# Kernel tuning notes

Measured on AMD Instinct MI355X. Metric: run time of the kernel, lower is better.

Reference implementation:

```python
import jax, jax.numpy as jnp
import numpy as np

N_NODES = 50000
N_EDGES = 1600000
D_IN = 256
HEADS = 4
SUB_IN = 64   # generate_sub_head_nums(256, 4) -> [64, 64, 64, 64]
SUB_H = 64    # hidden_dim // head_num


def setup_inputs() -> dict:
    key = jax.random.key(0)
    k1, k2, k3 = jax.random.split(key, 3)
    x = jax.random.normal(k1, (N_NODES, D_IN), dtype=jnp.float32)
    edge_index = jax.random.randint(k2, (2, N_EDGES), 0, N_NODES, dtype=jnp.int64)
    # per-head GCNConv weights: glorot-ish scale
    W = jax.random.normal(k3, (HEADS, SUB_IN, SUB_H), dtype=jnp.float32) * (1.0 / np.sqrt(SUB_IN))
    b = jnp.zeros((HEADS, SUB_H), dtype=jnp.float32)
    return {"x": x, "edge_index": edge_index, "W": W, "b": b}


def _gcn_aggregate(x_sub, edge_index, n_nodes):
    """Symmetric-normalized aggregation with self-loops: D^-1/2 (A+I) D^-1/2 x_sub."""
    row, col = edge_index[0], edge_index[1]          # source -> target
    loops = jnp.arange(n_nodes, dtype=row.dtype)
    row2 = jnp.concatenate([row, loops])
    col2 = jnp.concatenate([col, loops])
    deg = jax.ops.segment_sum(jnp.ones_like(col2, dtype=x_sub.dtype), col2,
                              num_segments=n_nodes)
    dinv = jnp.where(deg > 0, jax.lax.rsqrt(deg), 0.0)
    norm = dinv[row2] * dinv[col2]                   # [E+N]
    msgs = x_sub[row2] * norm[:, None]               # [E+N, SUB_IN] gather
    return jax.ops.segment_sum(msgs, col2, num_segments=n_nodes)  # [N, SUB_IN] scatter


def reference(x, edge_index, W, b):
    n = x.shape[0]
    # Faithful to source bug: `start` never advances, so every head reads x[:, 0:SUB_IN].
    x0 = x[:, :SUB_IN]                               # [N, 64], shared by all heads
    # aggregation is linear -> aggregate once, then apply per-head linear (same math as GCNConv(xW))
    agg = _gcn_aggregate(x0, edge_index, n)          # [N, 64]
    heads = jax.nn.relu(jnp.einsum('nf,hfo->nho', agg, W) + b[None, :, :])  # [N, H, SUB_H]
    x_cat = heads.reshape(n, HEADS * SUB_H)          # concat over heads along last dim
    return x_cat, heads
```

## Files before the change

### kernel.cpp

```cpp
#include <hip/hip_runtime.h>
#include <hip/hip_bf16.h>

#define NNODES 50000
#define NEDGES 1600000
#define NBIN2  1564
#define CAPB2  1440
#define SCAP   320
#define OVFCAP 65536
#define BCHUNK 2000
#define NBBLK  800

__device__ __forceinline__ float bf2f(unsigned short u) {
    union { unsigned int i; float f; } x; x.i = ((unsigned int)u) << 16; return x.f;
}

__global__ __launch_bounds__(256) void k_bin(const int* __restrict__ edges,
                                             int* __restrict__ bincur,
                                             int* __restrict__ ovfcnt,
                                             int* __restrict__ ovf,
                                             int* __restrict__ binned) {
    __shared__ int pk[BCHUNK];
    __shared__ int hist[NBIN2];
    __shared__ int gbase[NBIN2];
    __shared__ int lcnt[NBIN2];
    int t = threadIdx.x;
    int e0 = blockIdx.x * BCHUNK;
    unsigned xcd;
    asm volatile("s_getreg_b32 %0, hwreg(HW_REG_XCC_ID)" : "=s"(xcd));
    xcd &= 7;
    for (int i = t; i < NBIN2; i += 256) { hist[i] = 0; lcnt[i] = 0; }
    __syncthreads();
    for (int i = t * 4; i < BCHUNK; i += 1024) {
        int4 r4 = *(const int4*)&edges[e0 + i];
        int4 c4 = *(const int4*)&edges[NEDGES + e0 + i];
        int b0 = c4.x >> 5, b1 = c4.y >> 5, b2 = c4.z >> 5, b3 = c4.w >> 5;
        pk[i + 0] = r4.x | ((c4.x & 31) << 16) | (b0 << 21);
        pk[i + 1] = r4.y | ((c4.y & 31) << 16) | (b1 << 21);
        pk[i + 2] = r4.z | ((c4.z & 31) << 16) | (b2 << 21);
        pk[i + 3] = r4.w | ((c4.w & 31) << 16) | (b3 << 21);
        atomicAdd(&hist[b0], 1);
        atomicAdd(&hist[b1], 1);
        atomicAdd(&hist[b2], 1);
        atomicAdd(&hist[b3], 1);
    }
    __syncthreads();
    for (int i = t; i < NBIN2; i += 256) {
        int h = hist[i];
        gbase[i] = (h > 0) ? atomicAdd(&bincur[xcd * NBIN2 + i], h) : 0;
    }
    __syncthreads();
    for (int i = t; i < BCHUNK; i += 256) {
        int v = pk[i];
        int bin = ((unsigned)v) >> 21;
        int p = gbase[bin] + atomicAdd(&lcnt[bin], 1);
        if (p < SCAP) {
            binned[(xcd * NBIN2 + bin) * SCAP + p] = v;
        } else {
            int op = atomicAdd(ovfcnt, 1);
            if (op < OVFCAP) ovf[op] = v;
        }
    }
}

__global__ __launch_bounds__(256) void k_sortbin(const int* __restrict__ bincur,
                                                 const int* __restrict__ binned,
                                                 const int* __restrict__ ovfcnt,
                                                 const int* __restrict__ ovf,
                                                 const float* __restrict__ x,
                                                 int* __restrict__ rowptr,
                                                 int* __restrict__ cntn,
                                                 float* __restrict__ dinv,
                                                 unsigned short* __restrict__ x0s,
                                                 int* __restrict__ csr) {
    __shared__ int h[32];
    __shared__ int off[32];
    __shared__ int cur[32];
    __shared__ float dv[32];
    __shared__ int slen[8];
    __shared__ int stage[CAPB2];
    int t = threadIdx.x, bin = blockIdx.x;
    int wave = t >> 6, lane = t & 63;
    int n0 = bin * 32;
    float xv[8];
    #pragma unroll
    for (int k = 0; k < 8; ++k) {
        int n = n0 + wave + 4 * k;
        xv[k] = (n < NNODES) ? x[n * 256 + lane] : 0.0f;
    }
    if (t < 32) h[t] = 0;
    if (t < 8) slen[t] = min(bincur[t * NBIN2 + bin], SCAP);
    __syncthreads();
    int novf = ovfcnt[0];
    for (int sp = 0; sp < 8; sp += 2) {
        int s = sp + (t >> 7);
        int tl = t & 127;
        int len = slen[s];
        const int* __restrict__ bb = binned + (s * NBIN2 + bin) * SCAP;
        for (int e = tl; e < len; e += 128)
            atomicAdd(&h[(bb[e] >> 16) & 31], 1);
    }
    for (int e = t; e < novf; e += 256) {
        int v = ovf[e];
        if (((unsigned)v >> 21) == (unsigned)bin) atomicAdd(&h[(v >> 16) & 31], 1);
    }
    __syncthreads();
    if (t < 32) {
        int v = h[t];
        int inc = v;
        #pragma unroll
        for (int d = 1; d < 32; d <<= 1) {
            int u = __shfl_up(inc, d);
            if (lane >= d) inc += u;
        }
        int ex = inc - v;
        off[t] = ex;
        cur[t] = ex;
        float dc = rsqrtf((float)(v + 1));
        dv[t] = dc;
        int n = n0 + t;
        if (n < NNODES) {
            dinv[n] = dc;
            rowptr[n] = bin * CAPB2 + ex;
            cntn[n] = v;
        }
    }
    __syncthreads();
    for (int sp = 0; sp < 8; sp += 2) {
        int s = sp + (t >> 7);
        int tl = t & 127;
        int len = slen[s];
        const int* __restrict__ bb = binned + (s * NBIN2 + bin) * SCAP;
        for (int e = tl; e < len; e += 128) {
            int v = bb[e];
            int p = atomicAdd(&cur[(v >> 16) & 31], 1);
            if (p < CAPB2) stage[p] = v & 0xFFFF;
        }
    }
    for (int e = t; e < novf; e += 256) {
        int v = ovf[e];
        if (((unsigned)v >> 21) == (unsigned)bin) {
            int p = atomicAdd(&cur[(v >> 16) & 31], 1);
            if (p < CAPB2) stage[p] = v & 0xFFFF;
        }
    }
    __syncthreads();
    int total = min(off[31] + h[31], CAPB2);
    for (int e = t; e < total; e += 256)
        csr[bin * CAPB2 + e] = stage[e];
    #pragma unroll
    for (int k = 0; k < 8; ++k) {
        int i = wave + 4 * k;
        int n = n0 + i;
        if (n < NNODES) {
            __hip_bfloat16 v = __float2bfloat16(xv[k] * dv[i]);
            x0s[n * 64 + lane] = *(unsigned short*)&v;
        }
    }
}

__global__ __launch_bounds__(256) void k_gather(const unsigned short* __restrict__ x0s,
                                                const int* __restrict__ rowptr,
                                                const int* __restrict__ cntn,
                                                const float* __restrict__ dinv,
                                                const int* __restrict__ csr,
                                                float* __restrict__ agg) {
    int wave = threadIdx.x >> 6, lane = threadIdx.x & 63;
    int n = blockIdx.x * 4 + wave;
    int start = rowptr[n], len = cntn[n];
    float acc0 = bf2f(x0s[n * 64 + lane]);
    float acc1 = 0.0f;
    for (int base = 0; base < len; base += 64) {
        int m = min(len - base, 64);
        int idx = (lane < m) ? csr[start + base + lane] : 0;
        int j = 0;
        for (; j + 8 <= m; j += 8) {
            int r0 = __shfl(idx, j + 0), r1 = __shfl(idx, j + 1);
            int r2 = __shfl(idx, j + 2), r3 = __shfl(idx, j + 3);
            int r4 = __shfl(idx, j + 4), r5 = __shfl(idx, j + 5);
            int r6 = __shfl(idx, j + 6), r7 = __shfl(idx, j + 7);
            float f0 = bf2f(x0s[r0 * 64 + lane]);
            float f1 = bf2f(x0s[r1 * 64 + lane]);
            float f2 = bf2f(x0s[r2 * 64 + lane]);
            float f3 = bf2f(x0s[r3 * 64 + lane]);
            float f4 = bf2f(x0s[r4 * 64 + lane]);
            float f5 = bf2f(x0s[r5 * 64 + lane]);
            float f6 = bf2f(x0s[r6 * 64 + lane]);
            float f7 = bf2f(x0s[r7 * 64 + lane]);
            acc0 += (f0 + f1) + (f2 + f3);
            acc1 += (f4 + f5) + (f6 + f7);
        }
        for (; j < m; ++j) {
            int r = __shfl(idx, j);
            acc0 += bf2f(x0s[r * 64 + lane]);
        }
    }
    agg[n * 64 + lane] = (acc0 + acc1) * dinv[n];
}

__global__ __launch_bounds__(256) void k_gemm(const float* __restrict__ agg,
                                              const float* __restrict__ W,
                                              const float* __restrict__ b,
                                              float* __restrict__ out0,
                                              float* __restrict__ out1) {
    int t = threadIdx.x;
    int h = t >> 6, o = t & 63;
    float wreg[64];
    #pragma unroll
    for (int f = 0; f < 64; ++f) wreg[f] = W[h * 4096 + f * 64 + o];
    float bias = b[t];
    int n0 = blockIdx.x * 25;
    for (int i = 0; i < 25; ++i) {
        int n = n0 + i;
        const float* __restrict__ arow = agg + n * 64;
        float acc = bias;
        #pragma unroll
        for (int f = 0; f < 64; ++f) acc = fmaf(arow[f], wreg[f], acc);
        float v = fmaxf(acc, 0.0f);
        __builtin_nontemporal_store(v, &out0[n * 256 + t]);
        __builtin_nontemporal_store(v, &out1[n * 256 + t]);
    }
}


extern "C" void kernel_launch(void* const* d_in, const int* in_sizes, int n_in,
                              void* d_out, int out_size, void* d_ws, size_t ws_size,
                              hipStream_t stream) {
    const float* x     = (const float*)d_in[0];
    const int*   edges = (const int*)d_in[1];
    const float* W     = (const float*)d_in[2];
    const float* b     = (const float*)d_in[3];

    float* out0 = (float*)d_out;
    float* out1 = out0 + (size_t)NNODES * 256;

    char* ws = (char*)d_ws;
    int*            bincur = (int*)(ws + 0);
    int*            ovfcnt = (int*)(ws + 50176);
    int*            ovf    = (int*)(ws + 50688);
    float*          dinv   = (float*)(ws + 312832);
    int*            rowptr = (int*)(ws + 513024);
    int*            cntn   = (int*)(ws + 713216);
    int*            binned = (int*)(ws + 913408);
    int*            csr    = (int*)(ws + 16928768);
    unsigned short* x0s    = (unsigned short*)(ws + 25937408);
    float*          agg    = (float*)(ws + 32337408);

    hipMemsetAsync(ws, 0, 50180, stream);
    k_bin    <<<NBBLK, 256, 0, stream>>>(edges, bincur, ovfcnt, ovf, binned);
    k_sortbin<<<NBIN2, 256, 0, stream>>>(bincur, binned, ovfcnt, ovf, x, rowptr, cntn, dinv, x0s, csr);
    k_gather <<<NNODES / 4, 256, 0, stream>>>(x0s, rowptr, cntn, dinv, csr, agg);
    k_gemm   <<<2000, 256, 0, stream>>>(agg, W, b, out0, out1);
}
```

Baseline: 244.5 us.

## Split bf16 feature table into two 32-column halves gathered in separate passes

```diff
diff --git a/kernel.cpp b/kernel.cpp
--- a/kernel.cpp
+++ b/kernel.cpp
@@ -9,6 +9,7 @@
 #define OVFCAP 65536
 #define BCHUNK 2000
 #define NBBLK  800
+#define HALFSZ (NNODES * 32)
 
 __device__ __forceinline__ float bf2f(unsigned short u) {
     union { unsigned int i; float f; } x; x.i = ((unsigned int)u) << 16; return x.f;
@@ -153,7 +154,7 @@
         int n = n0 + i;
         if (n < NNODES) {
             __hip_bfloat16 v = __float2bfloat16(xv[k] * dv[i]);
-            x0s[n * 64 + lane] = *(unsigned short*)&v;
+            x0s[(lane >> 5) * HALFSZ + n * 32 + (lane & 31)] = *(unsigned short*)&v;
         }
     }
 }
@@ -163,38 +164,42 @@
                                                 const int* __restrict__ cntn,
                                                 const float* __restrict__ dinv,
                                                 const int* __restrict__ csr,
-                                                float* __restrict__ agg) {
-    int wave = threadIdx.x >> 6, lane = threadIdx.x & 63;
-    int n = blockIdx.x * 4 + wave;
+                                                float* __restrict__ agg,
+                                                int pass) {
+    const unsigned short* __restrict__ xh = x0s + pass * HALFSZ;
+    int t = threadIdx.x, lane = t & 63, w = t >> 6;
+    int half = lane >> 5, fi = lane & 31;
+    int n = (blockIdx.x * 4 + w) * 2 + half;
     int start = rowptr[n], len = cntn[n];
-    float acc0 = bf2f(x0s[n * 64 + lane]);
+    float acc0 = bf2f(xh[n * 32 + fi]);
     float acc1 = 0.0f;
-    for (int base = 0; base < len; base += 64) {
-        int m = min(len - base, 64);
-        int idx = (lane < m) ? csr[start + base + lane] : 0;
+    for (int base = 0; base < len; base += 32) {
+        int m = min(len - base, 32);
+        int idx = (fi < m) ? __builtin_nontemporal_load(&csr[start + base + fi]) : 0;
         int j = 0;
         for (; j + 8 <= m; j += 8) {
-            int r0 = __shfl(idx, j + 0), r1 = __shfl(idx, j + 1);
-            int r2 = __shfl(idx, j + 2), r3 = __shfl(idx, j + 3);
-            int r4 = __shfl(idx, j + 4), r5 = __shfl(idx, j + 5);
-            int r6 = __shfl(idx, j + 6), r7 = __shfl(idx, j + 7);
-            float f0 = bf2f(x0s[r0 * 64 + lane]);
-            float f1 = bf2f(x0s[r1 * 64 + lane]);
-            float f2 = bf2f(x0s[r2 * 64 + lane]);
-            float f3 = bf2f(x0s[r3 * 64 + lane]);
-            float f4 = bf2f(x0s[r4 * 64 + lane]);
-            float f5 = bf2f(x0s[r5 * 64 + lane]);
-            float f6 = bf2f(x0s[r6 * 64 + lane]);
-            float f7 = bf2f(x0s[r7 * 64 + lane]);
+            int r0 = __shfl(idx, j + 0, 32), r1 = __shfl(idx, j + 1, 32);
+            int r2 = __shfl(idx, j + 2, 32), r3 = __shfl(idx, j + 3, 32);
+            int r4 = __shfl(idx, j + 4, 32), r5 = __shfl(idx, j + 5, 32);
+            int r6 = __shfl(idx, j + 6, 32), r7 = __shfl(idx, j + 7, 32);
+            float f0 = bf2f(xh[r0 * 32 + fi]);
+            float f1 = bf2f(xh[r1 * 32 + fi]);
+            float f2 = bf2f(xh[r2 * 32 + fi]);
+            float f3 = bf2f(xh[r3 * 32 + fi]);
+            float f4 = bf2f(xh[r4 * 32 + fi]);
+            float f5 = bf2f(xh[r5 * 32 + fi]);
+            float f6 = bf2f(xh[r6 * 32 + fi]);
+            float f7 = bf2f(xh[r7 * 32 + fi]);
             acc0 += (f0 + f1) + (f2 + f3);
             acc1 += (f4 + f5) + (f6 + f7);
         }
         for (; j < m; ++j) {
-            int r = __shfl(idx, j);
-            acc0 += bf2f(x0s[r * 64 + lane]);
-        }
-    }
-    agg[n * 64 + lane] = (acc0 + acc1) * dinv[n];
+            int r = __shfl(idx, j, 32);
+            acc0 += bf2f(xh[r * 32 + fi]);
+        }
+    }
+    float v = (acc0 + acc1) * dinv[n];
+    __builtin_nontemporal_store(v, &agg[n * 64 + pass * 32 + fi]);
 }
 
 __global__ __launch_bounds__(256) void k_gemm(const float* __restrict__ agg,
@@ -248,6 +253,7 @@
     hipMemsetAsync(ws, 0, 50180, stream);
     k_bin    <<<NBBLK, 256, 0, stream>>>(edges, bincur, ovfcnt, ovf, binned);
     k_sortbin<<<NBIN2, 256, 0, stream>>>(bincur, binned, ovfcnt, ovf, x, rowptr, cntn, dinv, x0s, csr);
-    k_gather <<<NNODES / 4, 256, 0, stream>>>(x0s, rowptr, cntn, dinv, csr, agg);
+    k_gather <<<6250, 256, 0, stream>>>(x0s, rowptr, cntn, dinv, csr, agg, 0);
+    k_gather <<<6250, 256, 0, stream>>>(x0s, rowptr, cntn, dinv, csr, agg, 1);
     k_gemm   <<<2000, 256, 0, stream>>>(agg, W, b, out0, out1);
 }
```

New measurement: 280.1 us. +14.6%, slower.

## Split gather into two feature-half passes with packed bf16x2 loads

Applied to the files above, without the earlier changes.

```diff
diff --git a/kernel.cpp b/kernel.cpp
--- a/kernel.cpp
+++ b/kernel.cpp
@@ -163,38 +163,57 @@
                                                 const int* __restrict__ cntn,
                                                 const float* __restrict__ dinv,
                                                 const int* __restrict__ csr,
-                                                float* __restrict__ agg) {
+                                                float* __restrict__ agg,
+                                                int pass) {
+    const unsigned int* __restrict__ xu = (const unsigned int*)x0s;
     int wave = threadIdx.x >> 6, lane = threadIdx.x & 63;
+    int q = lane >> 4, fi = lane & 15;
+    int off = pass * 16 + fi;
     int n = blockIdx.x * 4 + wave;
     int start = rowptr[n], len = cntn[n];
-    float acc0 = bf2f(x0s[n * 64 + lane]);
-    float acc1 = 0.0f;
+    float dc = dinv[n];
+    float acc0 = 0.0f, acc1 = 0.0f;
+    unsigned int sv = xu[n * 32 + off];
+    if (q == 0) { acc0 = bf2f((unsigned short)sv); acc1 = bf2f((unsigned short)(sv >> 16)); }
     for (int base = 0; base < len; base += 64) {
         int m = min(len - base, 64);
         int idx = (lane < m) ? csr[start + base + lane] : 0;
         int j = 0;
-        for (; j + 8 <= m; j += 8) {
-            int r0 = __shfl(idx, j + 0), r1 = __shfl(idx, j + 1);
-            int r2 = __shfl(idx, j + 2), r3 = __shfl(idx, j + 3);
-            int r4 = __shfl(idx, j + 4), r5 = __shfl(idx, j + 5);
-            int r6 = __shfl(idx, j + 6), r7 = __shfl(idx, j + 7);
-            float f0 = bf2f(x0s[r0 * 64 + lane]);
-            float f1 = bf2f(x0s[r1 * 64 + lane]);
-            float f2 = bf2f(x0s[r2 * 64 + lane]);
-            float f3 = bf2f(x0s[r3 * 64 + lane]);
-            float f4 = bf2f(x0s[r4 * 64 + lane]);
-            float f5 = bf2f(x0s[r5 * 64 + lane]);
-            float f6 = bf2f(x0s[r6 * 64 + lane]);
-            float f7 = bf2f(x0s[r7 * 64 + lane]);
-            acc0 += (f0 + f1) + (f2 + f3);
-            acc1 += (f4 + f5) + (f6 + f7);
+        for (; j + 16 <= m; j += 16) {
+            int ra = __shfl(idx, j + q);
+            int rb = __shfl(idx, j + 4 + q);
+            int rc = __shfl(idx, j + 8 + q);
+            int rd = __shfl(idx, j + 12 + q);
+            unsigned int ua = xu[ra * 32 + off];
+            unsigned int ub = xu[rb * 32 + off];
+            unsigned int uc = xu[rc * 32 + off];
+            unsigned int ud = xu[rd * 32 + off];
+            acc0 += (bf2f((unsigned short)ua) + bf2f((unsigned short)ub))
+                  + (bf2f((unsigned short)uc) + bf2f((unsigned short)ud));
+            acc1 += (bf2f((unsigned short)(ua >> 16)) + bf2f((unsigned short)(ub >> 16)))
+                  + (bf2f((unsigned short)(uc >> 16)) + bf2f((unsigned short)(ud >> 16)));
+        }
+        for (; j + 4 <= m; j += 4) {
+            int ra = __shfl(idx, j + q);
+            unsigned int ua = xu[ra * 32 + off];
+            acc0 += bf2f((unsigned short)ua);
+            acc1 += bf2f((unsigned short)(ua >> 16));
         }
         for (; j < m; ++j) {
             int r = __shfl(idx, j);
-            acc0 += bf2f(x0s[r * 64 + lane]);
-        }
-    }
-    agg[n * 64 + lane] = (acc0 + acc1) * dinv[n];
+            if (q == 0) {
+                unsigned int u = xu[r * 32 + off];
+                acc0 += bf2f((unsigned short)u);
+                acc1 += bf2f((unsigned short)(u >> 16));
+            }
+        }
+    }
+    acc0 += __shfl_xor(acc0, 16); acc0 += __shfl_xor(acc0, 32);
+    acc1 += __shfl_xor(acc1, 16); acc1 += __shfl_xor(acc1, 32);
+    if (lane < 16) {
+        float2 v = make_float2(acc0 * dc, acc1 * dc);
+        *(float2*)&agg[n * 64 + pass * 32 + 2 * fi] = v;
+    }
 }
 
 __global__ __launch_bounds__(256) void k_gemm(const float* __restrict__ agg,
@@ -248,6 +267,7 @@
     hipMemsetAsync(ws, 0, 50180, stream);
     k_bin    <<<NBBLK, 256, 0, stream>>>(edges, bincur, ovfcnt, ovf, binned);
     k_sortbin<<<NBIN2, 256, 0, stream>>>(bincur, binned, ovfcnt, ovf, x, rowptr, cntn, dinv, x0s, csr);
-    k_gather <<<NNODES / 4, 256, 0, stream>>>(x0s, rowptr, cntn, dinv, csr, agg);
+    k_gather <<<NNODES / 4, 256, 0, stream>>>(x0s, rowptr, cntn, dinv, csr, agg, 0);
+    k_gather <<<NNODES / 4, 256, 0, stream>>>(x0s, rowptr, cntn, dinv, csr, agg, 1);
     k_gemm   <<<2000, 256, 0, stream>>>(agg, W, b, out0, out1);
 }
```

Measured after the change: 260.2 us. 6.4% more time.
